# Kernel tuning notes

Measured on AMD Instinct MI355X. Metric: run time of the kernel, lower is better.

Reference implementation:

```python
import jax, jax.numpy as jnp
import numpy as np

N_NODES = 50000
N_EDGES = 800000
INPUT_DIM = 8
HIDDEN_DIM = 128


def setup_inputs() -> dict:
    key = jax.random.key(0)
    k = jax.random.split(key, 8)
    x = jax.random.normal(k[0], (N_NODES, INPUT_DIM), dtype=jnp.float32)
    edge_index = jax.random.randint(k[1], (2, N_EDGES), 0, N_NODES, dtype=jnp.int64)
    edge_attr = jax.random.uniform(k[2], (N_EDGES, 1), dtype=jnp.float32)
    node_embedding = jax.random.normal(k[3], (N_NODES, HIDDEN_DIM), dtype=jnp.float32)
    # Linear weights stored as [in, out] so y = x @ W (bias=False everywhere)
    s1 = 1.0 / np.sqrt(INPUT_DIM)
    sh = 1.0 / np.sqrt(HIDDEN_DIM)
    W1 = jax.random.uniform(k[4], (INPUT_DIM, HIDDEN_DIM), jnp.float32, -s1, s1)
    W2 = jax.random.uniform(k[5], (HIDDEN_DIM, HIDDEN_DIM), jnp.float32, -sh, sh)
    W3 = jax.random.uniform(k[6], (HIDDEN_DIM, HIDDEN_DIM), jnp.float32, -sh, sh)
    W4 = jax.random.uniform(k[7], (1, HIDDEN_DIM), jnp.float32, -1.0, 1.0)
    return {"x": x, "edge_index": edge_index, "edge_attr": edge_attr,
            "node_embedding": node_embedding, "W1": W1, "W2": W2, "W3": W3, "W4": W4}


def reference(x, edge_index, edge_attr, node_embedding, W1, W2, W3, W4):
    n = x.shape[0]
    row, col = edge_index[0], edge_index[1]
    # theta_1(x): [N, hidden]
    node_feature_embedding = x @ W1
    # gather neighbor embeddings along edges, scatter-sum to destination rows
    node_embedding_aggr = jax.ops.segment_sum(node_embedding[col], row, num_segments=n)
    # relu(theta_4(edge_attr)): [E, hidden], then scatter-sum to rows
    edge_feature_embedding = jax.nn.relu(edge_attr @ W4)
    edge_embedding_aggr = jax.ops.segment_sum(edge_feature_embedding, row, num_segments=n)
    return jax.nn.relu(node_feature_embedding + node_embedding_aggr @ W2 + edge_embedding_aggr @ W3)
```

## Files before the change

kernel.cpp:

```cpp
#include <hip/hip_runtime.h>

#define N_NODES 50000
#define N_EDGES 800000
#define IN_DIM  8
#define HD      128
#define N_SCAN_BLOCKS ((N_NODES + 255) / 256)
#define NREP 16
#define NTILES ((N_NODES + 63) / 64)
#define N_HIST_BLOCKS (N_EDGES / 256)
#define HIST_PER_BLOCK 4
#define GRID_P1 (NTILES * 2)
#define ZERO_INT4 ((NREP * N_NODES + 256) / 4)
#define N_ZERO_BLOCKS ((ZERO_INT4 + 255) / 256)
#define GRID_PREP (N_ZERO_BLOCKS + 2)

typedef unsigned short ushort_t;
typedef unsigned int uint_t;
typedef __attribute__((ext_vector_type(8))) short short8;
typedef __attribute__((ext_vector_type(4))) float float4v;
typedef __attribute__((ext_vector_type(4))) int int4v;
typedef __attribute__((ext_vector_type(2))) uint_t uint2v;

static __device__ inline unsigned short f2bf(float f) {
    unsigned u = __float_as_uint(f);
    unsigned r = (u + 0x7FFF + ((u >> 16) & 1)) >> 16;
    return (unsigned short)r;
}
static __device__ inline float bf2f(unsigned short b) {
    return __uint_as_float(((unsigned)b) << 16);
}

__global__ void prep_kernel(const float* __restrict__ W2,
                            short8* __restrict__ blob,
                            int* __restrict__ cnt,
                            const float* __restrict__ W4,
                            const float* __restrict__ W3,
                            float* __restrict__ v3) {
    int b = blockIdx.x;
    int t = threadIdx.x;
    if (b < N_ZERO_BLOCKS) {
        int idx = b * 256 + t;
        if (idx < ZERO_INT4) {
            int4v z = {0, 0, 0, 0};
            ((int4v*)cnt)[idx] = z;
        }
        return;
    }
    if (b == N_ZERO_BLOCKS) {
#pragma unroll
        for (int i = 0; i < 8; ++i) {
            int slot = t * 8 + i;
            int f    = slot >> 6;
            int lane = slot & 63;
            int ct = f >> 2, ki = f & 3;
            int n16 = lane & 15, quad = lane >> 4;
            short8 fr;
#pragma unroll
            for (int j = 0; j < 8; ++j) {
                int k = ki * 32 + quad * 8 + j;
                fr[j] = (short)f2bf(W2[k * HD + ct * 16 + n16]);
            }
            blob[slot] = fr;
        }
        return;
    }
    if (t < HD) {
        float acc = 0.f;
        for (int k = 0; k < HD; ++k) {
            float w = W4[k];
            w = w > 0.f ? w : 0.f;
            acc += w * W3[k * HD + t];
        }
        v3[t] = acc;
    }
}

__global__ __launch_bounds__(256, 2)
void phase1_kernel(const float* __restrict__ emb,
                   const short8* __restrict__ blob,
                   ushort_t* __restrict__ T16,
                   const int* __restrict__ ei,
                   int* __restrict__ cnt,
                   ushort_t* __restrict__ rank16) {
    if (blockIdx.x & 1) {
        int hb = blockIdx.x >> 1;
        int c0 = hb * HIST_PER_BLOCK;
        int r[HIST_PER_BLOCK];
#pragma unroll
        for (int q = 0; q < HIST_PER_BLOCK; ++q) {
            int c = c0 + q;
            r[q] = (c < N_HIST_BLOCKS) ? ei[c * 256 + threadIdx.x] : -1;
        }
        int rk[HIST_PER_BLOCK];
#pragma unroll
        for (int q = 0; q < HIST_PER_BLOCK; ++q)
            if (r[q] >= 0)
                rk[q] = atomicAdd(
                    &cnt[((c0 + q) & (NREP - 1)) * N_NODES + r[q]], 1);
#pragma unroll
        for (int q = 0; q < HIST_PER_BLOCK; ++q)
            if (r[q] >= 0)
                rank16[(c0 + q) * 256 + threadIdx.x] = (ushort_t)rk[q];
        return;
    }

    int tt   = blockIdx.x >> 1;
    int t    = threadIdx.x;
    int wave = t >> 6;
    int lane = t & 63;
    int n16  = lane & 15;
    int quad = lane >> 4;

    short8 wfrag[8][4];
#pragma unroll
    for (int ct = 0; ct < 8; ++ct)
#pragma unroll
        for (int ki = 0; ki < 4; ++ki)
            wfrag[ct][ki] = blob[(ct * 4 + ki) * 64 + lane];

    int rowbase = tt * 64 + wave * 16;
    int row  = rowbase + n16;
    int rowc = row < N_NODES ? row : N_NODES - 1;
    const float4v* arow = (const float4v*)(emb + (size_t)rowc * HD);

    short8 efrag[4];
#pragma unroll
    for (int ki = 0; ki < 4; ++ki) {
        float4v lo = __builtin_nontemporal_load(&arow[ki * 8 + quad * 2]);
        float4v hi = __builtin_nontemporal_load(&arow[ki * 8 + quad * 2 + 1]);
        short8 a;
        a[0] = (short)f2bf(lo[0]); a[1] = (short)f2bf(lo[1]);
        a[2] = (short)f2bf(lo[2]); a[3] = (short)f2bf(lo[3]);
        a[4] = (short)f2bf(hi[0]); a[5] = (short)f2bf(hi[1]);
        a[6] = (short)f2bf(hi[2]); a[7] = (short)f2bf(hi[3]);
        efrag[ki] = a;
    }

    float4v acc[8];
#pragma unroll
    for (int ct = 0; ct < 8; ++ct) acc[ct] = (float4v){0.f, 0.f, 0.f, 0.f};

#pragma unroll
    for (int ki = 0; ki < 4; ++ki)
#pragma unroll
        for (int ct = 0; ct < 8; ++ct)
            acc[ct] = __builtin_amdgcn_mfma_f32_16x16x32_bf16(
                wfrag[ct][ki], efrag[ki], acc[ct], 0, 0, 0);

    if (row < N_NODES) {
        ushort_t* dstu = T16 + (size_t)row * HD + quad * 4;
#pragma unroll
        for (int ct = 0; ct < 8; ++ct) {
            uint2v v;
            v[0] = (uint_t)f2bf(acc[ct][0]) | ((uint_t)f2bf(acc[ct][1]) << 16);
            v[1] = (uint_t)f2bf(acc[ct][2]) | ((uint_t)f2bf(acc[ct][3]) << 16);
            *(uint2v*)(dstu + ct * 16) = v;
        }
    }
}

__global__ void scan1_kernel(const int* __restrict__ cnt,
                             int* __restrict__ off,
                             int* __restrict__ bases,
                             int* __restrict__ bsums) {
    __shared__ int lds[256];
    int t = threadIdx.x;
    int n = blockIdx.x * 256 + t;
    int c[NREP];
    int tsum = 0;
#pragma unroll
    for (int r = 0; r < NREP; ++r) {
        c[r] = (n < N_NODES) ? cnt[r * N_NODES + n] : 0;
        tsum += c[r];
    }
    lds[t] = tsum;
    __syncthreads();
    for (int o = 1; o < 256; o <<= 1) {
        int add = (t >= o) ? lds[t - o] : 0;
        __syncthreads();
        lds[t] += add;
        __syncthreads();
    }
    int ex = lds[t] - tsum;
    int total = lds[255];
    if (n < N_NODES) {
        off[n] = ex;
        int run = ex;
#pragma unroll
        for (int r = 0; r < NREP; ++r) {
            bases[r * N_NODES + n] = run;
            run += c[r];
        }
    }
    for (int bb = blockIdx.x + 1 + t; bb < N_SCAN_BLOCKS; bb += 256)
        atomicAdd(&bsums[bb], total);
}

__global__ void fill_kernel(const int* __restrict__ ei,
                            const float* __restrict__ attr,
                            const ushort_t* __restrict__ rank16,
                            const int* __restrict__ bases,
                            const int* __restrict__ bsums,
                            uint_t* __restrict__ packed) {
    int e = blockIdx.x * 256 + threadIdx.x;
    int rep = (e >> 8) & (NREP - 1);
    int r = ei[e];
    int pos = bases[rep * N_NODES + r] + bsums[r >> 8] + (int)rank16[e];
    uint_t p = ((uint_t)f2bf(attr[e]) << 16) | (uint_t)ei[N_EDGES + e];
    packed[pos] = p;
}

__global__ void aggregate_kernel(const int* __restrict__ off,
                                 const int* __restrict__ bsums,
                                 const uint_t* __restrict__ packed,
                                 const ushort_t* __restrict__ T16,
                                 const float* __restrict__ x,
                                 const float* __restrict__ W1,
                                 const float* __restrict__ v3,
                                 float* __restrict__ out) {
    int tid  = blockIdx.x * 256 + threadIdx.x;
    int node = tid >> 4;
    int lane = tid & 15;
    int s  = off[node] + bsums[node >> 8];
    int e1 = (node + 1 == N_NODES) ? N_EDGES
                                   : off[node + 1] + bsums[(node + 1) >> 8];
    int deg = e1 - s;

    float acc[8];
#pragma unroll
    for (int i = 0; i < 8; ++i) acc[i] = 0.f;
    float ssum = 0.f;

    for (int base = 0; base < deg; base += 16) {
        int rem = deg - base; if (rem > 16) rem = 16;
        uint_t p = 0;
        if (lane < rem) p = __builtin_nontemporal_load(&packed[s + base + lane]);
        ssum += __uint_as_float(p & 0xFFFF0000u);
        int col = (int)(p & 0xFFFFu);
        int j = 0;
        for (; j + 4 <= rem; j += 4) {
            int c0 = __shfl(col, j + 0, 16);
            int c1 = __shfl(col, j + 1, 16);
            int c2 = __shfl(col, j + 2, 16);
            int c3 = __shfl(col, j + 3, 16);
            short8 t0 = ((const short8*)(T16 + (size_t)c0 * HD))[lane];
            short8 t1 = ((const short8*)(T16 + (size_t)c1 * HD))[lane];
            short8 t2 = ((const short8*)(T16 + (size_t)c2 * HD))[lane];
            short8 t3 = ((const short8*)(T16 + (size_t)c3 * HD))[lane];
#pragma unroll
            for (int i = 0; i < 8; ++i)
                acc[i] += (bf2f((ushort_t)t0[i]) + bf2f((ushort_t)t1[i]))
                        + (bf2f((ushort_t)t2[i]) + bf2f((ushort_t)t3[i]));
        }
        for (; j < rem; ++j) {
            int c = __shfl(col, j, 16);
            short8 tv = ((const short8*)(T16 + (size_t)c * HD))[lane];
#pragma unroll
            for (int i = 0; i < 8; ++i)
                acc[i] += bf2f((ushort_t)tv[i]);
        }
    }
    for (int o = 8; o; o >>= 1) ssum += __shfl_xor(ssum, o, 16);

    const float4v* v3p = (const float4v*)v3;
    float4v b0 = v3p[lane * 2], b1 = v3p[lane * 2 + 1];
    acc[0] += ssum * b0[0]; acc[1] += ssum * b0[1];
    acc[2] += ssum * b0[2]; acc[3] += ssum * b0[3];
    acc[4] += ssum * b1[0]; acc[5] += ssum * b1[1];
    acc[6] += ssum * b1[2]; acc[7] += ssum * b1[3];
#pragma unroll
    for (int i = 0; i < IN_DIM; ++i) {
        float xi = x[node * IN_DIM + i];
        const float4v* wp = (const float4v*)(W1 + i * HD);
        float4v w0 = wp[lane * 2], w1 = wp[lane * 2 + 1];
        acc[0] += xi * w0[0]; acc[1] += xi * w0[1];
        acc[2] += xi * w0[2]; acc[3] += xi * w0[3];
        acc[4] += xi * w1[0]; acc[5] += xi * w1[1];
        acc[6] += xi * w1[2]; acc[7] += xi * w1[3];
    }
    float4v o0, o1;
    o0[0] = fmaxf(acc[0], 0.f); o0[1] = fmaxf(acc[1], 0.f);
    o0[2] = fmaxf(acc[2], 0.f); o0[3] = fmaxf(acc[3], 0.f);
    o1[0] = fmaxf(acc[4], 0.f); o1[1] = fmaxf(acc[5], 0.f);
    o1[2] = fmaxf(acc[6], 0.f); o1[3] = fmaxf(acc[7], 0.f);
    float4v* op = (float4v*)(out + (size_t)node * HD);
    __builtin_nontemporal_store(o0, op + lane * 2);
    __builtin_nontemporal_store(o1, op + lane * 2 + 1);
}

extern "C" void kernel_launch(void* const* d_in, const int* in_sizes, int n_in,
                              void* d_out, int out_size, void* d_ws, size_t ws_size,
                              hipStream_t stream) {
    const float* x    = (const float*)d_in[0];
    const int*   ei   = (const int*)  d_in[1];
    const float* attr = (const float*)d_in[2];
    const float* emb  = (const float*)d_in[3];
    const float* W1   = (const float*)d_in[4];
    const float* W2   = (const float*)d_in[5];
    const float* W3   = (const float*)d_in[6];
    const float* W4   = (const float*)d_in[7];
    float* out = (float*)d_out;

    char* w = (char*)d_ws;
    uint_t*   packed = (uint_t*)w;
    ushort_t* T16    = (ushort_t*)(w + (size_t)N_EDGES * 4);
    short8*   blob   = (short8*)((char*)T16 + (size_t)N_NODES * HD * 2);
    int*      off    = (int*)((char*)blob + 2048 * 16);
    int*      bases  = off + N_NODES + 4;
    int*      cnt    = bases + NREP * N_NODES;
    int*      bsums  = cnt + NREP * N_NODES;
    float*    v3     = (float*)(bsums + 256);
    ushort_t* rank16 = (ushort_t*)(v3 + HD);

    prep_kernel  <<<GRID_PREP, 256, 0, stream>>>(W2, blob, cnt, W4, W3, v3);
    phase1_kernel<<<GRID_P1, 256, 0, stream>>>(emb, blob, T16, ei, cnt, rank16);
    scan1_kernel <<<N_SCAN_BLOCKS, 256, 0, stream>>>(cnt, off, bases, bsums);
    fill_kernel  <<<N_HIST_BLOCKS, 256, 0, stream>>>(ei, attr, rank16, bases, bsums, packed);
    aggregate_kernel<<<(N_NODES * 16) / 256, 256, 0, stream>>>(
        off, bsums, packed, T16, x, W1, v3, out);
}
```

Before: 193.5 us.

## Build per-replica node histograms in LDS by node range instead of global atomics

The edge-row histogram now runs in LDS. Each of 128 blocks takes one replica and one node range (6250 nodes), scans that replica's edge chunks, and uses shared-memory atomics to assign ranks, then writes its counts straight to the global cnt array. This removes the global zeroing pass and the global atomics. The cost is that every block rereads its replica's edge rows 8 times (once per range), and the block now uses 25KB of LDS, which may lower occupancy for the co-resident GEMM tiles. The bsums reset moves into the prep kernel.

```diff
diff --git a/kernel.cpp b/kernel.cpp
--- a/kernel.cpp
+++ b/kernel.cpp
@@ -8,11 +8,11 @@
 #define NREP 16
 #define NTILES ((N_NODES + 63) / 64)
 #define N_HIST_BLOCKS (N_EDGES / 256)
-#define HIST_PER_BLOCK 4
-#define GRID_P1 (NTILES * 2)
-#define ZERO_INT4 ((NREP * N_NODES + 256) / 4)
-#define N_ZERO_BLOCKS ((ZERO_INT4 + 255) / 256)
-#define GRID_PREP (N_ZERO_BLOCKS + 2)
+#define NRANGE 8
+#define RANGE_N (N_NODES / NRANGE)
+#define N_HISTB (NREP * NRANGE)
+#define GRID_P1 (N_HISTB + NTILES)
+#define GRID_PREP 2
 
 typedef unsigned short ushort_t;
 typedef unsigned int uint_t;
@@ -32,21 +32,12 @@
 
 __global__ void prep_kernel(const float* __restrict__ W2,
                             short8* __restrict__ blob,
-                            int* __restrict__ cnt,
                             const float* __restrict__ W4,
                             const float* __restrict__ W3,
-                            float* __restrict__ v3) {
-    int b = blockIdx.x;
+                            float* __restrict__ v3,
+                            int* __restrict__ bsums) {
     int t = threadIdx.x;
-    if (b < N_ZERO_BLOCKS) {
-        int idx = b * 256 + t;
-        if (idx < ZERO_INT4) {
-            int4v z = {0, 0, 0, 0};
-            ((int4v*)cnt)[idx] = z;
-        }
-        return;
-    }
-    if (b == N_ZERO_BLOCKS) {
+    if (blockIdx.x == 0) {
 #pragma unroll
         for (int i = 0; i < 8; ++i) {
             int slot = t * 8 + i;
@@ -64,6 +55,7 @@
         }
         return;
     }
+    bsums[t] = 0;
     if (t < HD) {
         float acc = 0.f;
         for (int k = 0; k < HD; ++k) {
@@ -82,30 +74,41 @@
                    const int* __restrict__ ei,
                    int* __restrict__ cnt,
                    ushort_t* __restrict__ rank16) {
-    if (blockIdx.x & 1) {
-        int hb = blockIdx.x >> 1;
-        int c0 = hb * HIST_PER_BLOCK;
-        int r[HIST_PER_BLOCK];
-#pragma unroll
-        for (int q = 0; q < HIST_PER_BLOCK; ++q) {
-            int c = c0 + q;
-            r[q] = (c < N_HIST_BLOCKS) ? ei[c * 256 + threadIdx.x] : -1;
-        }
-        int rk[HIST_PER_BLOCK];
-#pragma unroll
-        for (int q = 0; q < HIST_PER_BLOCK; ++q)
-            if (r[q] >= 0)
-                rk[q] = atomicAdd(
-                    &cnt[((c0 + q) & (NREP - 1)) * N_NODES + r[q]], 1);
-#pragma unroll
-        for (int q = 0; q < HIST_PER_BLOCK; ++q)
-            if (r[q] >= 0)
-                rank16[(c0 + q) * 256 + threadIdx.x] = (ushort_t)rk[q];
+    __shared__ uint_t hcnt[RANGE_N];
+    int t = threadIdx.x;
+
+    if (blockIdx.x < N_HISTB) {
+        int rep   = blockIdx.x & (NREP - 1);
+        int range = blockIdx.x / NREP;
+        int rbase = range * RANGE_N;
+        for (int i = t; i < RANGE_N; i += 256) hcnt[i] = 0u;
+        __syncthreads();
+        int g    = t >> 6;
+        int lane = t & 63;
+        int NC = (N_HIST_BLOCKS - rep + NREP - 1) / NREP;
+        for (int j0 = 0; j0 < NC; j0 += 4) {
+            int j = j0 + g;
+            if (j < NC) {
+                int c  = rep + j * NREP;
+                int e0 = c * 256 + lane * 4;
+                int4v rv = *(const int4v*)(ei + e0);
+#pragma unroll
+                for (int q = 0; q < 4; ++q) {
+                    int lr = rv[q] - rbase;
+                    if ((unsigned)lr < (unsigned)RANGE_N) {
+                        uint_t rk = atomicAdd(&hcnt[lr], 1u);
+                        rank16[e0 + q] = (ushort_t)rk;
+                    }
+                }
+            }
+        }
+        __syncthreads();
+        int* crow = cnt + rep * N_NODES + rbase;
+        for (int i = t; i < RANGE_N; i += 256) crow[i] = (int)hcnt[i];
         return;
     }
 
-    int tt   = blockIdx.x >> 1;
-    int t    = threadIdx.x;
+    int tt   = blockIdx.x - N_HISTB;
     int wave = t >> 6;
     int lane = t & 63;
     int n16  = lane & 15;
@@ -312,7 +315,7 @@
     float*    v3     = (float*)(bsums + 256);
     ushort_t* rank16 = (ushort_t*)(v3 + HD);
 
-    prep_kernel  <<<GRID_PREP, 256, 0, stream>>>(W2, blob, cnt, W4, W3, v3);
+    prep_kernel  <<<GRID_PREP, 256, 0, stream>>>(W2, blob, W4, W3, v3, bsums);
     phase1_kernel<<<GRID_P1, 256, 0, stream>>>(emb, blob, T16, ei, cnt, rank16);
     scan1_kernel <<<N_SCAN_BLOCKS, 256, 0, stream>>>(cnt, off, bases, bsums);
     fill_kernel  <<<N_HIST_BLOCKS, 256, 0, stream>>>(ei, attr, rank16, bases, bsums, packed);
```

Result: faster. 180.1 us (-6.9%).
